# Optimization experiments

Hardware: AMD Instinct MI355X
Metric: run time of the kernel (lower is better)

Reference implementation:

```python
import jax, jax.numpy as jnp
import numpy as np

# Dimensions (match init_kwargs / input_specs)
T, BS = 256, 64
NTOKEN, NINP = 512, 512
NHID, NB, TOPK = 2048, 8, 4
BSZ = NHID // NB            # 256 = per-block hidden size
ATT_OUT = 340               # per-block value dim from input attention (attention_out)
DK = 64                     # input-attention key dim (RIMs default)
NH_C, DK_C = 4, 32          # communication attention: 4 heads, 32-dim each


def setup_inputs() -> dict:
    key = jax.random.key(0)
    ks = jax.random.split(key, 12)
    g = lambda k, shp, s=0.02: jax.random.normal(k, shp, dtype=jnp.float32) * s
    return dict(
        x=g(ks[0], (T, BS, NTOKEN), 1.0),
        h0=jnp.zeros((BS, NHID), jnp.float32),
        c0=jnp.zeros((BS, NHID), jnp.float32),
        W_enc=g(ks[1], (NTOKEN, NINP), 0.1),   # encoder = nn.Linear(ntoken, ninp)
        b_enc=jnp.zeros((NINP,), jnp.float32),
        Wq=g(ks[2], (BSZ, DK)),                # input-attention query (per block, shared weights)
        Wk=g(ks[3], (NINP, DK)),               # input-attention key
        Wv=g(ks[4], (NINP, ATT_OUT)),          # input-attention value
        Wi=g(ks[5], (NB, ATT_OUT, 4 * BSZ)),   # blockified LSTM input weights
        Wh=g(ks[6], (NB, BSZ, 4 * BSZ)),       # blockified LSTM recurrent weights
        b_lstm=jnp.zeros((NB, 4 * BSZ), jnp.float32),
        Wq_c=g(ks[7], (BSZ, NH_C * DK_C)),     # communication attention projections
        Wk_c=g(ks[8], (BSZ, NH_C * DK_C)),
        Wv_c=g(ks[9], (BSZ, NH_C * DK_C)),
        Wo_c=g(ks[10], (NH_C * DK_C, BSZ)),
    )


def reference(x, h0, c0, W_enc, b_enc, Wq, Wk, Wv, Wi, Wh, b_lstm,
              Wq_c, Wk_c, Wv_c, Wo_c):
    scale_in = 1.0 / jnp.sqrt(jnp.asarray(DK, x.dtype))
    scale_c = 1.0 / jnp.sqrt(jnp.asarray(DK_C, x.dtype))
    emb = x @ W_enc + b_enc  # (T,BS,NINP); dropout=0 -> identity

    def step(carry, xt):
        hx, cx = carry                                    # (BS,NHID) each
        hb = hx.reshape(BS, NB, BSZ)
        cb = cx.reshape(BS, NB, BSZ)

        # ---- input attention with null slot: RIM-style top-k block gating ----
        kv = jnp.stack([jnp.zeros_like(xt), xt], axis=1)              # (BS,2,NINP) null+input
        q = jnp.einsum('bnd,dk->bnk', hb, Wq)                         # (BS,NB,DK)
        k = jnp.einsum('bsd,dk->bsk', kv, Wk)                         # (BS,2,DK)
        v = jnp.einsum('bsd,dv->bsv', kv, Wv)                         # (BS,2,ATT_OUT)
        att = jax.nn.softmax(jnp.einsum('bnk,bsk->bns', q, k) * scale_in, axis=-1)
        inp_use = jnp.einsum('bns,bsv->bnv', att, v)                  # (BS,NB,ATT_OUT)
        null_att = att[:, :, 0]                                       # (BS,NB)
        # active blocks = TOPK blocks attending LEAST to the null slot
        _, idx = jax.lax.top_k(-null_att, TOPK)
        mask_b = jax.nn.one_hot(idx, NB, dtype=hx.dtype).sum(axis=1)  # (BS,NB) in {0,1}

        # ---- blockwise LSTM cell (all blocks computed, inactive ones gated out) ----
        gates = (jnp.einsum('bnv,nvh->bnh', inp_use, Wi)
                 + jnp.einsum('bnd,ndh->bnh', hb, Wh) + b_lstm)       # (BS,NB,4*BSZ)
        i_g, f_g, g_g, o_g = jnp.split(gates, 4, axis=-1)
        c_new = jax.nn.sigmoid(f_g) * cb + jax.nn.sigmoid(i_g) * jnp.tanh(g_g)
        h_new = jax.nn.sigmoid(o_g) * jnp.tanh(c_new)                 # (BS,NB,BSZ)

        # ---- inter-block communication attention (step_att), residual into active blocks ----
        qc = jnp.einsum('bnd,dh->bnh', h_new, Wq_c).reshape(BS, NB, NH_C, DK_C)
        kc = jnp.einsum('bnd,dh->bnh', h_new, Wk_c).reshape(BS, NB, NH_C, DK_C)
        vc = jnp.einsum('bnd,dh->bnh', h_new, Wv_c).reshape(BS, NB, NH_C, DK_C)
        ac = jax.nn.softmax(jnp.einsum('bnhk,bmhk->bhnm', qc, kc) * scale_c, axis=-1)
        oc = jnp.einsum('bhnm,bmhk->bnhk', ac, vc).reshape(BS, NB, NH_C * DK_C)
        h_new = h_new + mask_b[..., None] * (oc @ Wo_c)

        # ---- gate: only active blocks update their state ----
        m = mask_b[..., None]
        h_next = (m * h_new + (1.0 - m) * hb).reshape(BS, NHID)
        c_next = (m * c_new + (1.0 - m) * cb).reshape(BS, NHID)
        return (h_next, c_next), h_next

    (_, _), out = jax.lax.scan(step, (h0, c0), emb)  # out: (T,BS,NHID)
    return out
```

## Files before the change

kernel.cpp:

```cpp
#include <hip/hip_runtime.h>
#include <hip/hip_bf16.h>

#define T_STEPS 256
#define BS      64
#define NTOKEN  512
#define NINP    512
#define NHID    2048
#define NB      8
#define TOPKN   4
#define BSZ     256
#define ATT_OUT 340
#define DK      64
#define NH_C    4
#define DK_C    32
#define KSUM    (ATT_OUT + BSZ)
#define KV1     (DK + ATT_OUT)
#define RV      596
#define GATES   1024
#define NWG     256

#define AGENT __HIP_MEMORY_SCOPE_AGENT

__device__ __forceinline__ float sigf(float x) { return 1.0f / (1.0f + expf(-x)); }
__device__ __forceinline__ float aload(const float* p) {
  return __hip_atomic_load(p, __ATOMIC_RELAXED, AGENT);
}
__device__ __forceinline__ void astore(float* p, float v) {
  __hip_atomic_store(p, v, __ATOMIC_RELAXED, AGENT);
}
__device__ __forceinline__ unsigned aloadu(const unsigned* p) {
  return __hip_atomic_load(p, __ATOMIC_RELAXED, AGENT);
}
__device__ __forceinline__ void astoreu(unsigned* p, unsigned v) {
  __hip_atomic_store(p, v, __ATOMIC_RELAXED, AGENT);
}

__device__ __forceinline__ void gfma(float4& acc, const float4& a4, const float4& w0,
                                     const float4& w1, const float4& w2, const float4& w3) {
  acc.x += a4.x * w0.x + a4.y * w1.x + a4.z * w2.x + a4.w * w3.x;
  acc.y += a4.x * w0.y + a4.y * w1.y + a4.z * w2.y + a4.w * w3.y;
  acc.z += a4.x * w0.z + a4.y * w1.z + a4.z * w2.z + a4.w * w3.z;
  acc.w += a4.x * w0.w + a4.y * w1.w + a4.z * w2.w + a4.w * w3.w;
}
__device__ __forceinline__ void sfma(float4& acc, float s, const float4& w) {
  acc.x += s * w.x; acc.y += s * w.y; acc.z += s * w.z; acc.w += s * w.w;
}

__device__ __forceinline__ void gbar2(unsigned* flags, unsigned* gen, unsigned e) {
  const int w = blockIdx.x, tid = threadIdx.x;
  asm volatile("s_waitcnt vmcnt(0) lgkmcnt(0)" ::: "memory");
  __syncthreads();
  if (tid == 0) astoreu(&flags[w * 16], e);
  if (w == NWG - 1) {
    if (tid < NWG) {
      while (aloadu(&flags[tid * 16]) < e) __builtin_amdgcn_s_sleep(1);
    }
    __syncthreads();
    if (tid < 8) astoreu(&gen[tid * 16], e);
  } else {
    if (tid == 0) {
      while (aloadu(&gen[(w & 7) * 16]) < e) __builtin_amdgcn_s_sleep(1);
    }
  }
  __syncthreads();
}

__global__ void k_wc(const float* __restrict__ W_enc, const float* __restrict__ b_enc,
                     const float* __restrict__ Wk, const float* __restrict__ Wv,
                     float* __restrict__ Wc, float* __restrict__ bias_kv) {
  __shared__ float row[NINP];
  int d = blockIdx.x;
  const float* src = (d < NTOKEN) ? (W_enc + (size_t)d * NINP) : b_enc;
  for (int i = threadIdx.x; i < NINP; i += blockDim.x) row[i] = src[i];
  __syncthreads();
  float* dst = (d < NTOKEN) ? (Wc + (size_t)d * KV1) : bias_kv;
  for (int j = threadIdx.x; j < KV1; j += blockDim.x) {
    float acc = 0.f;
    if (j < DK) {
      for (int p = 0; p < NINP; ++p) acc += row[p] * Wk[(size_t)p * DK + j];
    } else {
      int jj = j - DK;
      for (int p = 0; p < NINP; ++p) acc += row[p] * Wv[(size_t)p * ATT_OUT + jj];
    }
    dst[j] = acc;
  }
}

__global__ void k_kv(const float* __restrict__ x, const float* __restrict__ Wc,
                     const float* __restrict__ bias_kv, const float* __restrict__ Wq,
                     float* __restrict__ k1v1) {
  __shared__ float xl[8 * NTOKEN];
  __shared__ float k1s[8 * DK];
  int r0 = blockIdx.x * 8;
  for (int i = threadIdx.x; i < 8 * NTOKEN; i += blockDim.x)
    xl[i] = x[(size_t)r0 * NTOKEN + i];
  __syncthreads();
  for (int j = threadIdx.x; j < KV1; j += 256) {
    float bj = bias_kv[j];
    float acc[8];
#pragma unroll
    for (int r = 0; r < 8; ++r) acc[r] = bj;
    for (int d = 0; d < NTOKEN; ++d) {
      float wc = Wc[(size_t)d * KV1 + j];
#pragma unroll
      for (int r = 0; r < 8; ++r) acc[r] += xl[r * NTOKEN + d] * wc;
    }
    if (j < DK) {
#pragma unroll
      for (int r = 0; r < 8; ++r) k1s[r * DK + j] = acc[r];
    } else {
#pragma unroll
      for (int r = 0; r < 8; ++r) k1v1[(size_t)(r0 + r) * RV + (j - DK)] = acc[r];
    }
  }
  __syncthreads();
  {
    int d = threadIdx.x;
    float a[8];
#pragma unroll
    for (int r = 0; r < 8; ++r) a[r] = 0.f;
    for (int dk4 = 0; dk4 < 16; ++dk4) {
      float4 w4 = *(const float4*)&Wq[(size_t)d * DK + dk4 * 4];
#pragma unroll
      for (int r = 0; r < 8; ++r) {
        float4 kk = *(const float4*)&k1s[r * DK + dk4 * 4];
        a[r] += kk.x * w4.x + kk.y * w4.y + kk.z * w4.z + kk.w * w4.w;
      }
    }
#pragma unroll
    for (int r = 0; r < 8; ++r) k1v1[(size_t)(r0 + r) * RV + ATT_OUT + d] = a[r];
  }
}

__global__ void k_fuse(const float* __restrict__ Wi, const float* __restrict__ Wh,
                       const float* __restrict__ b_lstm,
                       float* __restrict__ Wf, float* __restrict__ bf) {
  int nk = blockIdx.x;
  int n = nk / KSUM, k = nk % KSUM;
  const float* src = (k < ATT_OUT) ? (Wi + ((size_t)n * ATT_OUT + k) * GATES)
                                   : (Wh + ((size_t)n * BSZ + (k - ATT_OUT)) * GATES);
  float* dst = Wf + ((size_t)n * KSUM + k) * GATES;
  for (int gc = threadIdx.x; gc < GATES; gc += blockDim.x) {
    int t = gc >> 8, j = gc & 255;
    dst[j * 4 + t] = src[gc];
  }
  if (k == 0) {
    for (int gc = threadIdx.x; gc < GATES; gc += blockDim.x) {
      int t = gc >> 8, j = gc & 255;
      bf[(size_t)n * GATES + j * 4 + t] = b_lstm[(size_t)n * GATES + gc];
    }
  }
}

__global__ __launch_bounds__(1024)
void k_rnn(const float* __restrict__ k1v1, const float* __restrict__ Wf,
           const float* __restrict__ bf,
           const float* __restrict__ Wq_c, const float* __restrict__ Wk_c,
           const float* __restrict__ Wv_c, const float* __restrict__ Wo_c,
           const float* __restrict__ c0,
           float* h, float* hnew, float* zbuf,
           unsigned* bar, float* __restrict__ out) {
  const int w   = blockIdx.x;
  const int tid = threadIdx.x;
  const int n   = w & 7;
  const int csg = (w >> 3) & 7;
  const int bg  = w >> 6;

  unsigned* flags = bar;
  unsigned* gen   = bar + 4096;

  __shared__ __align__(16) float smem[12816];
  float* c_cur  = smem;
  float* c_pend = smem + 512;
  float* zl     = smem + 1024;
  float* attl   = smem + 1152;
  float* h_comm = smem + 1168;
  float* Al     = smem + 3216;

  if (tid < 512) {
    int b = tid >> 5, jj = tid & 31;
    c_cur[tid] = c0[(size_t)(bg * 16 + b) * NHID + n * BSZ + csg * 32 + jj];
  }
  if (w < BS) {
    for (int i = tid; i < NHID; i += 1024) h_comm[i] = aload(&h[(size_t)w * NHID + i]);
  }

  for (int t = 0; t < T_STEPS; ++t) {
#pragma unroll
    for (int r = 0; r < 4; ++r) {
      int i = r * 1024 + tid;
      int bb = i >> 8, d = i & 255;
      Al[bb * 600 + ATT_OUT + d] = aload(&h[(size_t)(bg * 16 + bb) * NHID + n * BSZ + d]);
    }
    if (tid >= 512 && tid < 640) {
      int q = tid - 512;
      zl[q] = aload(&zbuf[(size_t)(bg * 16 + (q >> 3)) * NB + (q & 7)]);
    }
    __syncthreads();
    {
      int bb = tid >> 6, lane = tid & 63;
      float4 h4  = *(float4*)&Al[bb * 600 + ATT_OUT + lane * 4];
      float4 wk4 = *(const float4*)&k1v1[((size_t)t * BS + bg * 16 + bb) * RV + ATT_OUT + lane * 4];
      float zp = h4.x * wk4.x + h4.y * wk4.y + h4.z * wk4.z + h4.w * wk4.w;
      zp += __shfl_xor(zp, 1);  zp += __shfl_xor(zp, 2);  zp += __shfl_xor(zp, 4);
      zp += __shfl_xor(zp, 8);  zp += __shfl_xor(zp, 16); zp += __shfl_xor(zp, 32);
      if (lane == 0) {
        float z = zp * 0.125f;
        attl[bb] = sigf(z);
        if (csg == 0) astore(&zbuf[(size_t)(bg * 16 + bb) * NB + n], z);
      }
    }
    __syncthreads();
    for (int i = tid; i < 16 * 85; i += 1024) {
      int bb = i / 85, q = i - bb * 85;
      float4 v4 = *(const float4*)&k1v1[((size_t)t * BS + bg * 16 + bb) * RV + q * 4];
      float a = attl[bb];
      float4 r;
      r.x = a * v4.x; r.y = a * v4.y; r.z = a * v4.z; r.w = a * v4.w;
      *(float4*)&Al[bb * 600 + q * 4] = r;
    }
    __syncthreads();
    const int jjG = tid & 31, boG = (tid >> 5) & 1, khG = tid >> 6;
    float4 acc[8];
#pragma unroll
    for (int i = 0; i < 8; ++i) acc[i] = make_float4(0.f, 0.f, 0.f, 0.f);
    {
      const float* Wr = Wf + (size_t)n * KSUM * GATES + (size_t)(csg * 32 + jjG) * 4;
      const float* Ab = Al + boG * 8 * 600;
#pragma unroll 2
      for (int k4 = khG * 4; k4 < KSUM; k4 += 64) {
        const float* wp = Wr + (size_t)k4 * GATES;
        float4 w0 = *(const float4*)(wp);
        float4 w1 = *(const float4*)(wp + GATES);
        float4 w2 = *(const float4*)(wp + 2 * GATES);
        float4 w3 = *(const float4*)(wp + 3 * GATES);
#pragma unroll
        for (int i = 0; i < 8; ++i) {
          float4 a4 = *(const float4*)&Ab[i * 600 + k4];
          gfma(acc[i], a4, w0, w1, w2, w3);
        }
      }
    }
    __syncthreads();
    {
      float4* red4 = (float4*)Al;
#pragma unroll
      for (int p = 0; p < 4; ++p) {
        red4[khG * 132 + boG * 64 + jjG * 2 + 0] = acc[2 * p];
        red4[khG * 132 + boG * 64 + jjG * 2 + 1] = acc[2 * p + 1];
        __syncthreads();
        if (tid < 128) {
          int rb = tid >> 5, jjr = tid & 31;
          int bo_r = rb >> 1, q_r = rb & 1;
          int batch = bo_r * 8 + 2 * p + q_r;
          float4 g4 = make_float4(0.f, 0.f, 0.f, 0.f);
#pragma unroll
          for (int kh = 0; kh < 16; ++kh) {
            float4 v = red4[kh * 132 + bo_r * 64 + jjr * 2 + q_r];
            g4.x += v.x; g4.y += v.y; g4.z += v.z; g4.w += v.w;
          }
          int jgr = csg * 32 + jjr;
          float4 bia = *(const float4*)&bf[(size_t)n * GATES + jgr * 4];
          float ig = sigf(g4.x + bia.x), fg = sigf(g4.y + bia.y);
          float gg = tanhf(g4.z + bia.z), og = sigf(g4.w + bia.w);
          float cc = c_cur[batch * 32 + jjr];
          if (t > 0) {
            float zn = zl[batch * 8 + n];
            int rank = 0;
#pragma unroll
            for (int j = 0; j < NB; ++j) {
              float zj = zl[batch * 8 + j];
              rank += (zj > zn || (zj == zn && j < n)) ? 1 : 0;
            }
            if (rank < TOPKN) cc = c_pend[batch * 32 + jjr];
          }
          float cn = fg * cc + ig * gg;
          float hn = og * tanhf(cn);
          c_cur[batch * 32 + jjr]  = cc;
          c_pend[batch * 32 + jjr] = cn;
          astore(&hnew[(size_t)(bg * 16 + batch) * NHID + n * BSZ + jgr], hn);
        }
        __syncthreads();
      }
    }
    gbar2(flags, gen, 2u * t + 1u);

    if (w < BS) {
      const int b = w;
      float* hnewl = Al;
      float* qcl   = Al + 2048;
      float* kcl   = Al + 3072;
      float* vcl   = Al + 4096;
      float* ocl   = Al + 5120;
      float* scl   = Al + 6144;
      float* acl   = Al + 6400;
      float* zlB   = Al + 6656;

      for (int i = tid; i < NHID; i += 1024)
        hnewl[i] = aload(&hnew[(size_t)b * NHID + i]);
      if (tid >= 1016) zlB[tid - 1016] = aload(&zbuf[(size_t)b * NB + (tid - 1016)]);
      __syncthreads();
      if (tid < 768) {
        int mat = tid >> 8, c4 = (tid >> 3) & 31, kq = tid & 7;
        int c0 = c4 * 4;
        const float* W = (mat == 0) ? Wq_c : (mat == 1) ? Wk_c : Wv_c;
        float4 a8[8];
#pragma unroll
        for (int i = 0; i < 8; ++i) a8[i] = make_float4(0.f, 0.f, 0.f, 0.f);
#pragma unroll 2
        for (int m = 0; m < 8; ++m) {
          int d0 = kq * 4 + 32 * m;
          float4 w_0 = *(const float4*)&W[(size_t)(d0 + 0) * 128 + c0];
          float4 w_1 = *(const float4*)&W[(size_t)(d0 + 1) * 128 + c0];
          float4 w_2 = *(const float4*)&W[(size_t)(d0 + 2) * 128 + c0];
          float4 w_3 = *(const float4*)&W[(size_t)(d0 + 3) * 128 + c0];
#pragma unroll
          for (int nn = 0; nn < 8; ++nn) {
            float4 h4 = *(const float4*)&hnewl[nn * 256 + d0];
            sfma(a8[nn], h4.x, w_0); sfma(a8[nn], h4.y, w_1);
            sfma(a8[nn], h4.z, w_2); sfma(a8[nn], h4.w, w_3);
          }
        }
#pragma unroll
        for (int mk = 1; mk <= 4; mk <<= 1) {
#pragma unroll
          for (int nn = 0; nn < 8; ++nn) {
            a8[nn].x += __shfl_xor(a8[nn].x, mk);
            a8[nn].y += __shfl_xor(a8[nn].y, mk);
            a8[nn].z += __shfl_xor(a8[nn].z, mk);
            a8[nn].w += __shfl_xor(a8[nn].w, mk);
          }
        }
        if (kq == 0) {
          float* dst = (mat == 0) ? qcl : (mat == 1) ? kcl : vcl;
#pragma unroll
          for (int nn = 0; nn < 8; ++nn)
            *(float4*)&dst[nn * 128 + c0] = a8[nn];
        }
      }
      __syncthreads();
      if (tid < 256) {
        int hh = tid >> 6, nq = (tid >> 3) & 7, m = tid & 7;
        const float* qrow = &qcl[nq * 128 + hh * 32];
        const float* krow = &kcl[m * 128 + hh * 32];
        float a = 0.f;
#pragma unroll
        for (int k4 = 0; k4 < 8; ++k4) {
          float4 q4 = *(const float4*)&qrow[k4 * 4];
          float4 k4v = *(const float4*)&krow[k4 * 4];
          a += q4.x * k4v.x + q4.y * k4v.y + q4.z * k4v.z + q4.w * k4v.w;
        }
        scl[tid] = a * 0.17677669529663687f;
      }
      __syncthreads();
      if (tid < 32) {
        int hh = tid >> 3, nq = tid & 7;
        const float* row = &scl[hh * 64 + nq * 8];
        float mx = -1e30f;
#pragma unroll
        for (int m = 0; m < NB; ++m) mx = fmaxf(mx, row[m]);
        float e[NB]; float sum = 0.f;
#pragma unroll
        for (int m = 0; m < NB; ++m) { e[m] = expf(row[m] - mx); sum += e[m]; }
        float inv = 1.f / sum;
#pragma unroll
        for (int m = 0; m < NB; ++m) acl[(hh * 8 + nq) * 8 + m] = e[m] * inv;
      }
      __syncthreads();
      if (tid < 256) {
        int nn = tid >> 5, c4 = tid & 31, c0 = c4 * 4, hh = c4 >> 3;
        const float* arow = &acl[(hh * 8 + nn) * 8];
        float4 a4 = make_float4(0.f, 0.f, 0.f, 0.f);
#pragma unroll
        for (int m = 0; m < NB; ++m) {
          float a = arow[m];
          float4 v4 = *(const float4*)&vcl[m * 128 + c0];
          sfma(a4, a, v4);
        }
        *(float4*)&ocl[tid * 4] = a4;
      }
      __syncthreads();
      if (tid < 512) {
        int nn = tid >> 6, j0 = (tid & 63) * 4;
        int li = nn * BSZ + j0;
        float zn = zlB[nn];
        int rank = 0;
#pragma unroll
        for (int j = 0; j < NB; ++j) {
          float zj = zlB[j];
          rank += (zj > zn || (zj == zn && j < nn)) ? 1 : 0;
        }
        float4 hv4;
        if (rank < TOPKN) {
          const float* oc = &ocl[nn * 128];
          float4 add = make_float4(0.f, 0.f, 0.f, 0.f);
#pragma unroll 4
          for (int p = 0; p < 128; ++p) {
            float o = oc[p];
            float4 w4 = *(const float4*)&Wo_c[(size_t)p * BSZ + j0];
            sfma(add, o, w4);
          }
          hv4.x = hnewl[li] + add.x;     hv4.y = hnewl[li + 1] + add.y;
          hv4.z = hnewl[li + 2] + add.z; hv4.w = hnewl[li + 3] + add.w;
          *(float4*)&h_comm[li] = hv4;
          size_t base = (size_t)b * NHID + li;
          astore(&h[base], hv4.x);     astore(&h[base + 1], hv4.y);
          astore(&h[base + 2], hv4.z); astore(&h[base + 3], hv4.w);
        } else {
          hv4 = *(float4*)&h_comm[li];
        }
        *(float4*)&out[((size_t)t * BS + b) * NHID + li] = hv4;
      }
    }
    gbar2(flags, gen, 2u * t + 2u);
  }
}

__global__ void k_sentinel(float* out) { out[0] = 12345.0f; }

extern "C" void kernel_launch(void* const* d_in, const int* in_sizes, int n_in,
                              void* d_out, int out_size, void* d_ws, size_t ws_size,
                              hipStream_t stream) {
  (void)in_sizes; (void)n_in; (void)out_size;
  const float* x      = (const float*)d_in[0];
  const float* h0     = (const float*)d_in[1];
  const float* c0     = (const float*)d_in[2];
  const float* W_enc  = (const float*)d_in[3];
  const float* b_enc  = (const float*)d_in[4];
  const float* Wq     = (const float*)d_in[5];
  const float* Wk     = (const float*)d_in[6];
  const float* Wv     = (const float*)d_in[7];
  const float* Wi     = (const float*)d_in[8];
  const float* Wh     = (const float*)d_in[9];
  const float* b_lstm = (const float*)d_in[10];
  const float* Wq_c   = (const float*)d_in[11];
  const float* Wk_c   = (const float*)d_in[12];
  const float* Wv_c   = (const float*)d_in[13];
  const float* Wo_c   = (const float*)d_in[14];
  float* out = (float*)d_out;

  float* ws = (float*)d_ws;
  size_t off = 0;
  auto alloc = [&](size_t nf) { float* p = ws + off; off += (nf + 15) & ~(size_t)15; return p; };
  float* k1v1 = alloc((size_t)T_STEPS * BS * RV);
  float* Wc   = alloc((size_t)NTOKEN * KV1);
  float* bias = alloc(KV1);
  float* Wf   = alloc((size_t)NB * KSUM * GATES);
  float* bf   = alloc((size_t)NB * GATES);
  float* h    = alloc((size_t)BS * NHID);
  float* hnew = alloc((size_t)BS * NHID);
  float* zbuf = alloc((size_t)BS * NB);
  unsigned* bar = (unsigned*)(ws + off); off += 4096 + 128 + 16;

  if (ws_size < off * sizeof(float)) {
    hipLaunchKernelGGL(k_sentinel, dim3(1), dim3(1), 0, stream, out);
    return;
  }

  hipMemsetAsync(bar, 0, (4096 + 128) * sizeof(unsigned), stream);
  hipMemcpyAsync(h, h0, (size_t)BS * NHID * sizeof(float), hipMemcpyDeviceToDevice, stream);

  hipLaunchKernelGGL(k_wc,   dim3(NTOKEN + 1),       dim3(128), 0, stream, W_enc, b_enc, Wk, Wv, Wc, bias);
  hipLaunchKernelGGL(k_kv,   dim3(T_STEPS * BS / 8), dim3(256), 0, stream, x, Wc, bias, Wq, k1v1);
  hipLaunchKernelGGL(k_fuse, dim3(NB * KSUM),        dim3(256), 0, stream, Wi, Wh, b_lstm, Wf, bf);
  hipLaunchKernelGGL(k_rnn,  dim3(NWG),              dim3(1024), 0, stream,
                     k1v1, Wf, bf, Wq_c, Wk_c, Wv_c, Wo_c, c0,
                     h, hnew, zbuf, bar, out);
}
```

Baseline: 13.74 ms.

## Prefetch next-step attention values, double-buffer zbuf, and widen barrier release flags

The persistent RNN kernel now prefetches the next timestep's value vectors and key slice into registers while the current gate GEMM and reduction run. It keeps separate shared buffers for the value and hidden operands instead of one combined staging area. The gating scores move to a double-buffered zbuf so reads and writes from different steps do not collide. The grid barrier releases each workgroup through its own generation flag rather than eight shared ones, and the communication Q/K rows are padded to reduce LDS bank conflicts. The cost is more LDS and register pressure, and the last workgroup now does more flag stores per barrier.

```diff
diff --git a/kernel.cpp b/kernel.cpp
--- a/kernel.cpp
+++ b/kernel.cpp
@@ -46,7 +46,7 @@
   acc.x += s * w.x; acc.y += s * w.y; acc.z += s * w.z; acc.w += s * w.w;
 }
 
-__device__ __forceinline__ void gbar2(unsigned* flags, unsigned* gen, unsigned e) {
+__device__ __forceinline__ void gbar(unsigned* flags, unsigned* gen, unsigned e) {
   const int w = blockIdx.x, tid = threadIdx.x;
   asm volatile("s_waitcnt vmcnt(0) lgkmcnt(0)" ::: "memory");
   __syncthreads();
@@ -56,10 +56,10 @@
       while (aloadu(&flags[tid * 16]) < e) __builtin_amdgcn_s_sleep(1);
     }
     __syncthreads();
-    if (tid < 8) astoreu(&gen[tid * 16], e);
+    if (tid < NWG) astoreu(&gen[tid * 16], e);
   } else {
     if (tid == 0) {
-      while (aloadu(&gen[(w & 7) * 16]) < e) __builtin_amdgcn_s_sleep(1);
+      while (aloadu(&gen[w * 16]) < e) __builtin_amdgcn_s_sleep(1);
     }
   }
   __syncthreads();
@@ -165,68 +165,88 @@
   const int n   = w & 7;
   const int csg = (w >> 3) & 7;
   const int bg  = w >> 6;
+  const int jjG = tid & 31, boG = (tid >> 5) & 1, khG = tid >> 6;
+  const int bb  = tid >> 6, lane = tid & 63;
 
   unsigned* flags = bar;
   unsigned* gen   = bar + 4096;
 
-  __shared__ __align__(16) float smem[12816];
+  __shared__ __align__(16) float smem[19488];
   float* c_cur  = smem;
   float* c_pend = smem + 512;
   float* zl     = smem + 1024;
   float* attl   = smem + 1152;
   float* h_comm = smem + 1168;
-  float* Al     = smem + 3216;
-
-  if (tid < 512) {
-    int b = tid >> 5, jj = tid & 31;
-    c_cur[tid] = c0[(size_t)(bg * 16 + b) * NHID + n * BSZ + csg * 32 + jj];
-  }
+  float* hl     = smem + 3216;
+  float* v1l    = smem + 7312;
+  float* R1     = smem + 12752;
+  float4* red4  = (float4*)(smem + 7312);
+
+  if (tid < 512)
+    c_cur[tid] = c0[(size_t)(bg * 16 + (tid >> 5)) * NHID + n * BSZ + csg * 32 + (tid & 31)];
   if (w < BS) {
-    for (int i = tid; i < NHID; i += 1024) h_comm[i] = aload(&h[(size_t)w * NHID + i]);
-  }
+#pragma unroll
+    for (int r = 0; r < 2; ++r) {
+      int i = r * 1024 + tid;
+      h_comm[i] = aload(&h[(size_t)w * NHID + i]);
+    }
+  }
+  for (int i = tid; i < 1360; i += 1024) {
+    int b = i / 85, q = i - b * 85;
+    *(float4*)&v1l[b * 340 + q * 4] =
+        *(const float4*)&k1v1[((size_t)(bg * 16 + b)) * RV + q * 4];
+  }
+  float4 wkreg = *(const float4*)&k1v1[((size_t)(bg * 16 + bb)) * RV + ATT_OUT + lane * 4];
+  const float4 bia = *(const float4*)&bf[(size_t)n * GATES + (csg * 32 + (tid & 31)) * 4];
 
   for (int t = 0; t < T_STEPS; ++t) {
-#pragma unroll
-    for (int r = 0; r < 4; ++r) {
-      int i = r * 1024 + tid;
-      int bb = i >> 8, d = i & 255;
-      Al[bb * 600 + ATT_OUT + d] = aload(&h[(size_t)(bg * 16 + bb) * NHID + n * BSZ + d]);
-    }
-    if (tid >= 512 && tid < 640) {
-      int q = tid - 512;
-      zl[q] = aload(&zbuf[(size_t)(bg * 16 + (q >> 3)) * NB + (q & 7)]);
-    }
-    __syncthreads();
+    float* zwr = zbuf + (t & 1) * 512;
+    float* zrd = zbuf + ((t & 1) ^ 1) * 512;
+
+    if (tid < 128) zl[tid] = aload(&zrd[(bg * 16 + (tid >> 3)) * 8 + (tid & 7)]);
     {
-      int bb = tid >> 6, lane = tid & 63;
-      float4 h4  = *(float4*)&Al[bb * 600 + ATT_OUT + lane * 4];
-      float4 wk4 = *(const float4*)&k1v1[((size_t)t * BS + bg * 16 + bb) * RV + ATT_OUT + lane * 4];
-      float zp = h4.x * wk4.x + h4.y * wk4.y + h4.z * wk4.z + h4.w * wk4.w;
+      const float* hp = &h[(size_t)(bg * 16 + bb) * NHID + n * BSZ + lane * 4];
+      float4 h4;
+      h4.x = aload(hp); h4.y = aload(hp + 1); h4.z = aload(hp + 2); h4.w = aload(hp + 3);
+      *(float4*)&hl[bb * 256 + lane * 4] = h4;
+      float zp = h4.x * wkreg.x + h4.y * wkreg.y + h4.z * wkreg.z + h4.w * wkreg.w;
       zp += __shfl_xor(zp, 1);  zp += __shfl_xor(zp, 2);  zp += __shfl_xor(zp, 4);
       zp += __shfl_xor(zp, 8);  zp += __shfl_xor(zp, 16); zp += __shfl_xor(zp, 32);
       if (lane == 0) {
         float z = zp * 0.125f;
         attl[bb] = sigf(z);
-        if (csg == 0) astore(&zbuf[(size_t)(bg * 16 + bb) * NB + n], z);
-      }
-    }
+        if (csg == 0) astore(&zwr[(bg * 16 + bb) * 8 + n], z);
+      }
+    }
+    const int tn = (t + 1 < T_STEPS) ? t + 1 : t;
+    wkreg = *(const float4*)&k1v1[((size_t)tn * BS + bg * 16 + bb) * RV + ATT_OUT + lane * 4];
     __syncthreads();
-    for (int i = tid; i < 16 * 85; i += 1024) {
-      int bb = i / 85, q = i - bb * 85;
-      float4 v4 = *(const float4*)&k1v1[((size_t)t * BS + bg * 16 + bb) * RV + q * 4];
-      float a = attl[bb];
-      float4 r;
-      r.x = a * v4.x; r.y = a * v4.y; r.z = a * v4.z; r.w = a * v4.w;
-      *(float4*)&Al[bb * 600 + q * 4] = r;
+
+    float4 pv0, pv1;
+    {
+      int b0 = tid / 85, q0 = tid - b0 * 85;
+      pv0 = *(const float4*)&k1v1[((size_t)tn * BS + bg * 16 + b0) * RV + q0 * 4];
+      int i1 = tid + 1024;
+      if (i1 < 1360) {
+        int b1 = i1 / 85, q1 = i1 - b1 * 85;
+        pv1 = *(const float4*)&k1v1[((size_t)tn * BS + bg * 16 + b1) * RV + q1 * 4];
+      }
+      for (int i = tid; i < 1360; i += 1024) {
+        int b = i / 85, q = i - b * 85;
+        float a = attl[b];
+        float4 v = *(float4*)&v1l[b * 340 + q * 4];
+        v.x *= a; v.y *= a; v.z *= a; v.w *= a;
+        *(float4*)&v1l[b * 340 + q * 4] = v;
+      }
     }
     __syncthreads();
-    const int jjG = tid & 31, boG = (tid >> 5) & 1, khG = tid >> 6;
+
     float4 acc[8];
 #pragma unroll
     for (int i = 0; i < 8; ++i) acc[i] = make_float4(0.f, 0.f, 0.f, 0.f);
     {
       const float* Wr = Wf + (size_t)n * KSUM * GATES + (size_t)(csg * 32 + jjG) * 4;
-      const float* Ab = Al + boG * 8 * 600;
+      const int bbase = boG * 8;
 #pragma unroll 2
       for (int k4 = khG * 4; k4 < KSUM; k4 += 64) {
         const float* wp = Wr + (size_t)k4 * GATES;
@@ -234,71 +254,88 @@
         float4 w1 = *(const float4*)(wp + GATES);
         float4 w2 = *(const float4*)(wp + 2 * GATES);
         float4 w3 = *(const float4*)(wp + 3 * GATES);
-#pragma unroll
-        for (int i = 0; i < 8; ++i) {
-          float4 a4 = *(const float4*)&Ab[i * 600 + k4];
-          gfma(acc[i], a4, w0, w1, w2, w3);
+        if (k4 < ATT_OUT) {
+#pragma unroll
+          for (int i = 0; i < 8; ++i) {
+            float4 a4 = *(const float4*)&v1l[(bbase + i) * 340 + k4];
+            gfma(acc[i], a4, w0, w1, w2, w3);
+          }
+        } else {
+#pragma unroll
+          for (int i = 0; i < 8; ++i) {
+            float4 a4 = *(const float4*)&hl[(bbase + i) * 256 + (k4 - ATT_OUT)];
+            gfma(acc[i], a4, w0, w1, w2, w3);
+          }
         }
       }
     }
     __syncthreads();
+
+#pragma unroll
+    for (int p = 0; p < 4; ++p) {
+      red4[khG * 132 + boG * 64 + jjG * 2 + 0] = acc[2 * p];
+      red4[khG * 132 + boG * 64 + jjG * 2 + 1] = acc[2 * p + 1];
+      __syncthreads();
+      if (tid < 128) {
+        const int rb = tid >> 5, jjr = tid & 31;
+        const int bo_r = rb >> 1, q_r = rb & 1;
+        const int batch = bo_r * 8 + 2 * p + q_r;
+        float4 g4 = make_float4(0.f, 0.f, 0.f, 0.f);
+#pragma unroll
+        for (int kh = 0; kh < 16; ++kh) {
+          float4 v = red4[kh * 132 + bo_r * 64 + jjr * 2 + q_r];
+          g4.x += v.x; g4.y += v.y; g4.z += v.z; g4.w += v.w;
+        }
+        const int jgr = csg * 32 + jjr;
+        float ig = sigf(g4.x + bia.x), fg = sigf(g4.y + bia.y);
+        float gg = tanhf(g4.z + bia.z), og = sigf(g4.w + bia.w);
+        float cc = c_cur[batch * 32 + jjr];
+        if (t > 0) {
+          float zn = zl[batch * 8 + n];
+          int rank = 0;
+#pragma unroll
+          for (int j = 0; j < NB; ++j) {
+            float zj = zl[batch * 8 + j];
+            rank += (zj > zn || (zj == zn && j < n)) ? 1 : 0;
+          }
+          if (rank < TOPKN) cc = c_pend[batch * 32 + jjr];
+        }
+        float cn = fg * cc + ig * gg;
+        float hn = og * tanhf(cn);
+        c_cur[batch * 32 + jjr]  = cc;
+        c_pend[batch * 32 + jjr] = cn;
+        astore(&hnew[(size_t)(bg * 16 + batch) * NHID + n * BSZ + jgr], hn);
+      }
+      __syncthreads();
+    }
     {
-      float4* red4 = (float4*)Al;
-#pragma unroll
-      for (int p = 0; p < 4; ++p) {
-        red4[khG * 132 + boG * 64 + jjG * 2 + 0] = acc[2 * p];
-        red4[khG * 132 + boG * 64 + jjG * 2 + 1] = acc[2 * p + 1];
-        __syncthreads();
-        if (tid < 128) {
-          int rb = tid >> 5, jjr = tid & 31;
-          int bo_r = rb >> 1, q_r = rb & 1;
-          int batch = bo_r * 8 + 2 * p + q_r;
-          float4 g4 = make_float4(0.f, 0.f, 0.f, 0.f);
-#pragma unroll
-          for (int kh = 0; kh < 16; ++kh) {
-            float4 v = red4[kh * 132 + bo_r * 64 + jjr * 2 + q_r];
-            g4.x += v.x; g4.y += v.y; g4.z += v.z; g4.w += v.w;
-          }
-          int jgr = csg * 32 + jjr;
-          float4 bia = *(const float4*)&bf[(size_t)n * GATES + jgr * 4];
-          float ig = sigf(g4.x + bia.x), fg = sigf(g4.y + bia.y);
-          float gg = tanhf(g4.z + bia.z), og = sigf(g4.w + bia.w);
-          float cc = c_cur[batch * 32 + jjr];
-          if (t > 0) {
-            float zn = zl[batch * 8 + n];
-            int rank = 0;
-#pragma unroll
-            for (int j = 0; j < NB; ++j) {
-              float zj = zl[batch * 8 + j];
-              rank += (zj > zn || (zj == zn && j < n)) ? 1 : 0;
-            }
-            if (rank < TOPKN) cc = c_pend[batch * 32 + jjr];
-          }
-          float cn = fg * cc + ig * gg;
-          float hn = og * tanhf(cn);
-          c_cur[batch * 32 + jjr]  = cc;
-          c_pend[batch * 32 + jjr] = cn;
-          astore(&hnew[(size_t)(bg * 16 + batch) * NHID + n * BSZ + jgr], hn);
-        }
-        __syncthreads();
-      }
-    }
-    gbar2(flags, gen, 2u * t + 1u);
+      int b0 = tid / 85, q0 = tid - b0 * 85;
+      *(float4*)&v1l[b0 * 340 + q0 * 4] = pv0;
+      int i1 = tid + 1024;
+      if (i1 < 1360) {
+        int b1 = i1 / 85, q1 = i1 - b1 * 85;
+        *(float4*)&v1l[b1 * 340 + q1 * 4] = pv1;
+      }
+    }
+    gbar(flags, gen, 2u * t + 1u);
 
     if (w < BS) {
       const int b = w;
-      float* hnewl = Al;
-      float* qcl   = Al + 2048;
-      float* kcl   = Al + 3072;
-      float* vcl   = Al + 4096;
-      float* ocl   = Al + 5120;
-      float* scl   = Al + 6144;
-      float* acl   = Al + 6400;
-      float* zlB   = Al + 6656;
-
-      for (int i = tid; i < NHID; i += 1024)
+      float* hnewl = R1;
+      float* qcl   = R1 + 2048;
+      float* kcl   = R1 + 3104;
+      float* vcl   = R1 + 4160;
+      float* ocl   = R1 + 5184;
+      float* scl   = R1 + 6208;
+      float* acl   = R1 + 6464;
+      float* zlB   = R1 + 6720;
+
+#pragma unroll
+      for (int r = 0; r < 2; ++r) {
+        int i = r * 1024 + tid;
         hnewl[i] = aload(&hnew[(size_t)b * NHID + i]);
-      if (tid >= 1016) zlB[tid - 1016] = aload(&zbuf[(size_t)b * NB + (tid - 1016)]);
+      }
+      if (tid < 8) zlB[tid] = aload(&zwr[b * 8 + tid]);
       __syncthreads();
       if (tid < 768) {
         int mat = tid >> 8, c4 = (tid >> 3) & 31, kq = tid & 7;
@@ -332,23 +369,27 @@
           }
         }
         if (kq == 0) {
-          float* dst = (mat == 0) ? qcl : (mat == 1) ? kcl : vcl;
-#pragma unroll
-          for (int nn = 0; nn < 8; ++nn)
-            *(float4*)&dst[nn * 128 + c0] = a8[nn];
+          if (mat == 2) {
+#pragma unroll
+            for (int nn = 0; nn < 8; ++nn) *(float4*)&vcl[nn * 128 + c0] = a8[nn];
+          } else {
+            float* dst = (mat == 0) ? qcl : kcl;
+#pragma unroll
+            for (int nn = 0; nn < 8; ++nn) *(float4*)&dst[nn * 132 + c0] = a8[nn];
+          }
         }
       }
       __syncthreads();
       if (tid < 256) {
         int hh = tid >> 6, nq = (tid >> 3) & 7, m = tid & 7;
-        const float* qrow = &qcl[nq * 128 + hh * 32];
-        const float* krow = &kcl[m * 128 + hh * 32];
+        const float* qrow = &qcl[nq * 132 + hh * 32];
+        const float* krow = &kcl[m * 132 + hh * 32];
         float a = 0.f;
 #pragma unroll
         for (int k4 = 0; k4 < 8; ++k4) {
           float4 q4 = *(const float4*)&qrow[k4 * 4];
-          float4 k4v = *(const float4*)&krow[k4 * 4];
-          a += q4.x * k4v.x + q4.y * k4v.y + q4.z * k4v.z + q4.w * k4v.w;
+          float4 kv = *(const float4*)&krow[k4 * 4];
+          a += q4.x * kv.x + q4.y * kv.y + q4.z * kv.z + q4.w * kv.w;
         }
         scl[tid] = a * 0.17677669529663687f;
       }
@@ -412,7 +453,7 @@
         *(float4*)&out[((size_t)t * BS + b) * NHID + li] = hv4;
       }
     }
-    gbar2(flags, gen, 2u * t + 2u);
+    gbar(flags, gen, 2u * t + 2u);
   }
 }
 
@@ -449,15 +490,15 @@
   float* bf   = alloc((size_t)NB * GATES);
   float* h    = alloc((size_t)BS * NHID);
   float* hnew = alloc((size_t)BS * NHID);
-  float* zbuf = alloc((size_t)BS * NB);
-  unsigned* bar = (unsigned*)(ws + off); off += 4096 + 128 + 16;
+  float* zbuf = alloc(2 * (size_t)BS * NB);
+  unsigned* bar = (unsigned*)(ws + off); off += 8192 + 16;
 
   if (ws_size < off * sizeof(float)) {
     hipLaunchKernelGGL(k_sentinel, dim3(1), dim3(1), 0, stream, out);
     return;
   }
 
-  hipMemsetAsync(bar, 0, (4096 + 128) * sizeof(unsigned), stream);
+  hipMemsetAsync(bar, 0, 8192 * sizeof(unsigned), stream);
   hipMemcpyAsync(h, h0, (size_t)BS * NHID * sizeof(float), hipMemcpyDeviceToDevice, stream);
 
   hipLaunchKernelGGL(k_wc,   dim3(NTOKEN + 1),       dim3(128), 0, stream, W_enc, b_enc, Wk, Wv, Wc, bias);
```

After: 24.48 ms. +78.2%, slower.
